# Kernel tuning notes

Hardware: AMD Instinct MI355X
Metric: run time of the kernel (lower is better)

The kernel has to match this reference:

```python
import jax, jax.numpy as jnp
import numpy as np

NUM_ITERS = 2  # quasi-DEER fixed-point iterations (module default num_iters=2)


def _affine_scan(A, b):
    """Parallel first-order linear recurrence h_t = A_t*h_{t-1} + b_t along axis=1.
    A, b: (B, T, H). Equivalent to torch accelerated-scan after removing pow-2 padding."""
    def comb(l, r):
        A1, b1 = l
        A2, b2 = r
        return A2 * A1, A2 * b1 + b2
    return jax.lax.associative_scan(comb, (A, b), axis=1)[1]


def _run_direction(x, W_in, b_in, W_rec, U_z, b_u, num_iters):
    """quasi-DEER evaluation of a MinRNN layer.
    x: (B, T, d_in). Returns states (B, T, H). Initial state h0 = 0 (hx=None)."""
    B, T, _ = x.shape
    H = b_in.shape[0]
    dtype = x.dtype
    h0 = jnp.zeros((B, H), dtype)
    diag_rec = jnp.diagonal(W_rec)  # (H,)
    # z depends only on the input, not on the state -> precompute once.
    z = jnp.tanh(jnp.einsum('bti,hi->bth', x, W_in) + b_in)  # (B, T, H)
    z0, z_rest = z[:, 0], z[:, 1:]
    states = jnp.zeros((B, T, H), dtype)
    for _ in range(num_iters):
        h_prev = states[:, :-1]  # (B, T-1, H), paired with inputs[:,1:]
        u = jax.nn.sigmoid(jnp.einsum('bth,gh->btg', h_prev, W_rec)
                           + jnp.einsum('bth,gh->btg', z_rest, U_z) + b_u)
        fs = u * h_prev + (1.0 - u) * z_rest                      # cell output f
        As = u + (h_prev - z_rest) * u * (1.0 - u) * diag_rec     # diagonal Jacobian
        bs = fs - As * h_prev
        u0 = jax.nn.sigmoid(h0 @ W_rec.T + z0 @ U_z.T + b_u)
        b0 = u0 * h0 + (1.0 - u0) * z0                            # f(x_0, h0)
        A = jnp.concatenate([jnp.zeros_like(b0)[:, None], As], axis=1)  # A0 = 0
        b = jnp.concatenate([b0[:, None], bs], axis=1)
        states = _affine_scan(A, b)
    return states


def _prnn_forward(input, Wf_in, bf_in, Wf_rec, Uf_z, bf_u,
                  Wb_in, bb_in, Wb_rec, Ub_z, bb_u):
    fwd = _run_direction(input, Wf_in, bf_in, Wf_rec, Uf_z, bf_u, NUM_ITERS)
    bwd = _run_direction(input[:, ::-1], Wb_in, bb_in, Wb_rec, Ub_z, bb_u, NUM_ITERS)[:, ::-1]
    output = jnp.concatenate([fwd, bwd], axis=2)      # (B, T, 2H)
    h_n = jnp.stack([fwd[:, -1], bwd[:, 0]])          # (2, B, H)
    return output, h_n


def setup_inputs() -> dict:
    key = jax.random.key(0)
    ks = jax.random.split(key, 12)
    B, T, D_IN, H = 8, 8192, 256, 256
    def minrnn_params(k0, k1, k2, d_in, h):
        kw, kr, ku = k0, k1, k2
        return dict(
            W_in=jax.random.normal(kw, (h, d_in), jnp.float32) / d_in ** 0.5,
            b_in=jnp.zeros((h,), jnp.float32),
            W_rec=jax.random.normal(kr, (h, h), jnp.float32) / h ** 0.5,
            U_z=jax.random.normal(ku, (h, h), jnp.float32) / h ** 0.5,
            b_u=jnp.zeros((h,), jnp.float32),
        )
    pf = minrnn_params(ks[0], ks[1], ks[2], D_IN, H)
    pb = minrnn_params(ks[3], ks[4], ks[5], D_IN, H)
    return {
        'input': jax.random.normal(ks[6], (B, T, D_IN), jnp.float32),
        'Wf_in': pf['W_in'], 'bf_in': pf['b_in'], 'Wf_rec': pf['W_rec'],
        'Uf_z': pf['U_z'], 'bf_u': pf['b_u'],
        'Wb_in': pb['W_in'], 'bb_in': pb['b_in'], 'Wb_rec': pb['W_rec'],
        'Ub_z': pb['U_z'], 'bb_u': pb['b_u'],
    }


def reference(input, Wf_in, bf_in, Wf_rec, Uf_z, bf_u,
              Wb_in, bb_in, Wb_rec, Ub_z, bb_u):
    return _prnn_forward(input, Wf_in, bf_in, Wf_rec, Uf_z, bf_u,
                         Wb_in, bb_in, Wb_rec, Ub_z, bb_u)
```

## Files before the change

### kernel.cpp

```cpp
#include <hip/hip_runtime.h>
#include <stdint.h>

typedef unsigned short u16;
typedef __attribute__((ext_vector_type(8))) short short8v;
typedef __attribute__((ext_vector_type(4))) short short4v;
typedef __attribute__((ext_vector_type(4))) float f32x4;

#define B_ 8
#define T_ 8192
#define H_ 256
#define M_ 65536
#define MH 16777216
#define NCH 256
#define CHL 32
#define NCHAN 4096

__device__ __forceinline__ u16 f2bf(float f) {
  union { float f; uint32_t u; } v; v.f = f;
  return (u16)((v.u + 0x7FFFu + ((v.u >> 16) & 1u)) >> 16);
}
__device__ __forceinline__ float bf2f(u16 s) {
  union { uint32_t u; float f; } v; v.u = ((uint32_t)s) << 16;
  return v.f;
}
__device__ __forceinline__ float sigm(float x) {
  return __fdividef(1.0f, 1.0f + __expf(-x));
}
__device__ __forceinline__ float tanhfast(float x) {
  return 1.0f - __fdividef(2.0f, __expf(2.0f * x) + 1.0f);
}

__device__ __forceinline__ void compute_Ab(float zf, float ag, float hp, float dr,
                                           float& Aa, float& bb) {
  const float u = sigm(ag);
  const float g = u * (1.f - u) * dr;
  Aa = u + (hp - zf) * g;
  bb = u * hp + (1.f - u) * zf - Aa * hp;
}

__global__ __launch_bounds__(256) void prep_kernel(
    const float* __restrict__ x, u16* __restrict__ xf,
    const float* __restrict__ w0, const float* __restrict__ w1, const float* __restrict__ w2,
    const float* __restrict__ w3, const float* __restrict__ w4, const float* __restrict__ w5,
    u16* __restrict__ wbf) {
  const int bx = blockIdx.x;
  const float* src;
  u16* dst;
  size_t i;
  if (bx < 8192) {
    i = ((size_t)bx * 256 + threadIdx.x) * 8;
    src = x; dst = xf;
  } else {
    const int r = bx - 8192;
    const int wsel = r >> 5, blk = r & 31;
    src = (wsel == 0) ? w0 : (wsel == 1) ? w1 : (wsel == 2) ? w2
        : (wsel == 3) ? w3 : (wsel == 4) ? w4 : w5;
    dst = wbf + (size_t)wsel * 65536;
    i = ((size_t)blk * 256 + threadIdx.x) * 8;
  }
  const float4* s4 = (const float4*)(src + i);
  float4 a = s4[0], b = s4[1];
  short8v o;
  o[0] = (short)f2bf(a.x); o[1] = (short)f2bf(a.y);
  o[2] = (short)f2bf(a.z); o[3] = (short)f2bf(a.w);
  o[4] = (short)f2bf(b.x); o[5] = (short)f2bf(b.y);
  o[6] = (short)f2bf(b.z); o[7] = (short)f2bf(b.w);
  *(short8v*)(dst + i) = o;
}

__device__ __forceinline__ void g2l16(const void* g, void* l) {
  __builtin_amdgcn_global_load_lds((const __attribute__((address_space(1))) void*)g,
                                   (__attribute__((address_space(3))) void*)l, 16, 0, 0);
}
__device__ __forceinline__ int ltswz(int row, int col16) {
  return row * 128 + (col16 ^ ((row & 7) << 4));
}

template <int EPI, int REVZ, int FUSE>
__global__ __launch_bounds__(256) void gemm_k(const u16* __restrict__ A, size_t strideA,
                                              const u16* __restrict__ Bw,
                                              const float* __restrict__ bias0,
                                              const float* __restrict__ bias1,
                                              const u16* addm, u16* C,
                                              const u16* zp_g,
                                              const float* __restrict__ Wf_rec,
                                              const float* __restrict__ Wb_rec,
                                              float* __restrict__ Pout,
                                              float* __restrict__ qout) {
  __shared__ __align__(16) char lds[32768];
  char* ldsA = lds;
  char* ldsB = lds + 16384;
  const int bz = blockIdx.z;
  A += (size_t)bz * strideA;
  Bw += (size_t)bz * 196608;
  C += (size_t)bz * (size_t)MH;
  if (EPI == 3) addm += (size_t)bz * (size_t)MH;
  if (FUSE == 2) zp_g += (size_t)bz * (size_t)MH;
  const float* bias = bz ? bias1 : bias0;

  const int tid = threadIdx.x;
  const int l = tid & 63, w = tid >> 6;
  const int tm = blockIdx.x, tn = blockIdx.y;
  const int m0 = (w >> 1) * 64, n0 = (w & 1) * 64;
  const int wbase = w * 1024;
  const bool rev = REVZ && (bz == 1);

  f32x4 vzero = {0.f, 0.f, 0.f, 0.f};
  f32x4 acc[4][4];
#pragma unroll
  for (int i = 0; i < 4; ++i)
#pragma unroll
    for (int j = 0; j < 4; ++j) acc[i][j] = vzero;

#pragma unroll
  for (int k0 = 0; k0 < 256; k0 += 64) {
#pragma unroll
    for (int is = 0; is < 4; ++is) {
      const int o = is * 4096 + tid * 16;
      const int row = o >> 7;
      const int cb = (o & 127) ^ ((row & 7) << 4);
      int rA = tm * 128 + row;
      if (rev) { int bb = rA >> 13; int t = rA & 8191; rA = (bb << 13) + (8191 - t); }
      const char* gA = (const char*)A + (size_t)rA * 512 + k0 * 2 + cb;
      g2l16(gA, ldsA + is * 4096 + wbase);
      const int rB = tn * 128 + row;
      const char* gB = (const char*)Bw + (size_t)rB * 512 + k0 * 2 + cb;
      g2l16(gB, ldsB + is * 4096 + wbase);
    }
    __syncthreads();
#pragma unroll
    for (int ks = 0; ks < 2; ++ks) {
      const int colb = (ks * 64 + (l >> 4) * 16) ^ ((l & 7) << 4);
      short8v av[4], bv[4];
#pragma unroll
      for (int i = 0; i < 4; ++i) {
        av[i] = *(const short8v*)(ldsA + (m0 + i * 16 + (l & 15)) * 128 + colb);
        bv[i] = *(const short8v*)(ldsB + (n0 + i * 16 + (l & 15)) * 128 + colb);
      }
#pragma unroll
      for (int i = 0; i < 4; ++i)
#pragma unroll
        for (int j = 0; j < 4; ++j)
          acc[i][j] = __builtin_amdgcn_mfma_f32_16x16x32_bf16(av[i], bv[j], acc[i][j], 0, 0, 0);
    }
    __syncthreads();
  }

  u16* lt = (u16*)lds;
  const int colL = n0 + (l & 15);
  const int rowL0 = m0 + ((l >> 4) << 2);
#pragma unroll
  for (int j = 0; j < 4; ++j) {
    const int cl = colL + j * 16;
    const int cg = tn * 128 + cl;
    const float bv = (EPI == 3) ? 0.f : bias[cg];
#pragma unroll
    for (int i = 0; i < 4; ++i)
#pragma unroll
      for (int r = 0; r < 4; ++r) {
        const int rl = rowL0 + i * 16 + r;
        float xv = acc[i][j][r] + bv;
        if (EPI == 3) xv += bf2f(addm[(size_t)(tm * 128 + rl) * 256 + cg]);
        if (EPI == 0) xv = tanhfast(xv);
        lt[ltswz(rl, cl)] = f2bf(xv);
      }
  }
  __syncthreads();
#pragma unroll
  for (int itr = 0; itr < 8; ++itr) {
    const int rl = w * 32 + itr * 4 + (l >> 4);
    const int c16 = ((l & 15) * 8) ^ ((rl & 7) << 4);
    short8v v = *(const short8v*)(lt + rl * 128 + c16);
    *(short8v*)((char*)C + (size_t)(tm * 128 + rl) * 512 + tn * 256 + (l & 15) * 16) = v;
  }

  if (FUSE) {
    const int cl = tid & 127;
    const int hg = tn * 128 + cl;
    const float dr = (bz ? Wb_rec : Wf_rec)[hg * 257];
    const int bb = (tm * 128) >> 13;
    const int c0 = ((tm * 128) & 8191) >> 5;
    const int ch = (bz * 8 + bb) * 256 + hg;
#pragma unroll
    for (int cc = 0; cc < 2; ++cc) {
      const int clc = (tid >> 7) * 2 + cc;
      float Pv = 1.f, qv = 0.f;
      const size_t gbase = (size_t)(tm * 128 + clc * CHL) * 256 + hg;
#pragma unroll 4
      for (int it = 0; it < CHL; ++it) {
        const float ag = bf2f(lt[ltswz(clc * CHL + it, cl)]);
        float zf, hp;
        if (FUSE == 1) { zf = bf2f(A[gbase + (size_t)it * 256]); hp = 0.f; }
        else { zf = bf2f(zp_g[gbase + (size_t)it * 256]); hp = bf2f(A[gbase + (size_t)it * 256]); }
        float Aa, bbv;
        compute_Ab(zf, ag, hp, dr, Aa, bbv);
        qv = Aa * qv + bbv;
        Pv *= Aa;
      }
      Pout[(size_t)(c0 + clc) * NCHAN + ch] = Pv;
      qout[(size_t)(c0 + clc) * NCHAN + ch] = qv;
    }
  }
}

__global__ __launch_bounds__(256) void scan_p2_kernel(const float* __restrict__ P,
                                                      const float* __restrict__ q,
                                                      float* __restrict__ hstart) {
  const int ch = blockIdx.x * 256 + threadIdx.x;
  float hs = 0.f;
#pragma unroll 8
  for (int c = 0; c < NCH; ++c) {
    hstart[c * NCHAN + ch] = hs;
    hs = P[c * NCHAN + ch] * hs + q[c * NCHAN + ch];
  }
}

template <int ITER>
__global__ __launch_bounds__(256) void scan_p3_kernel(
    const u16* __restrict__ zb, const u16* __restrict__ zub,
    const u16* __restrict__ s1b,
    const float* __restrict__ Wf_rec, const float* __restrict__ Wb_rec,
    const float* __restrict__ hstart,
    u16* __restrict__ s1out, float* __restrict__ out, float* __restrict__ hn) {
  const int wid = blockIdx.x * 4 + (threadIdx.x >> 6);
  const int lane = threadIdx.x & 63;
  const int c = wid & (NCH - 1);
  const int tmp = wid >> 8;
  const int b = tmp & 7;
  const int d = tmp >> 3;
  const int h0 = lane * 4;
  const float* Wr = d ? Wb_rec : Wf_rec;
  float dr[4];
#pragma unroll
  for (int j = 0; j < 4; ++j) dr[j] = Wr[(h0 + j) * 257];
  const size_t off = (size_t)d * MH + ((size_t)b * T_ + (size_t)c * CHL) * H_ + h0;
  const u16* zp = zb + off;
  const u16* zup = zub + off;
  const u16* s1p = s1b + off;
  const int ch0 = (d * 8 + b) * 256 + h0;
  f32x4 h4 = *(const f32x4*)(hstart + (size_t)c * NCHAN + ch0);
  float hc[4] = {h4[0], h4[1], h4[2], h4[3]};
  if (ITER == 1 && c == 0) {
    *(short4v*)(s1out + off) = (short4v){0, 0, 0, 0};
  }
#pragma unroll 4
  for (int it = 0; it < CHL; ++it) {
    const size_t ix = (size_t)it * H_;
    short4v z4 = *(const short4v*)(zp + ix);
    short4v a4 = *(const short4v*)(zup + ix);
    short4v s4 = {0, 0, 0, 0};
    if (ITER == 2) s4 = *(const short4v*)(s1p + ix);
#pragma unroll
    for (int j = 0; j < 4; ++j) {
      const float zf = bf2f((u16)z4[j]);
      const float ag = bf2f((u16)a4[j]);
      const float hp = (ITER == 2) ? bf2f((u16)s4[j]) : 0.f;
      float Aa, bb;
      compute_Ab(zf, ag, hp, dr[j], Aa, bb);
      hc[j] = Aa * hc[j] + bb;
    }
    const int t = c * CHL + it;
    if (ITER == 1) {
      if (t < T_ - 1) {
        short4v o = {(short)f2bf(hc[0]), (short)f2bf(hc[1]),
                     (short)f2bf(hc[2]), (short)f2bf(hc[3])};
        *(short4v*)(s1out + off + ix + H_) = o;
      }
    } else {
      const size_t to = (d == 0) ? ((size_t)b * T_ + t) * 512 + h0
                                 : ((size_t)b * T_ + (T_ - 1 - t)) * 512 + 256 + h0;
      *(f32x4*)(out + to) = (f32x4){hc[0], hc[1], hc[2], hc[3]};
      if (t == T_ - 1)
        *(f32x4*)(hn + (size_t)(d * 8 + b) * 256 + h0) = (f32x4){hc[0], hc[1], hc[2], hc[3]};
    }
  }
}

extern "C" void kernel_launch(void* const* d_in, const int* in_sizes, int n_in,
                              void* d_out, int out_size, void* d_ws, size_t ws_size,
                              hipStream_t stream) {
  const float* x      = (const float*)d_in[0];
  const float* Wf_in  = (const float*)d_in[1];
  const float* bf_in  = (const float*)d_in[2];
  const float* Wf_rec = (const float*)d_in[3];
  const float* Uf_z   = (const float*)d_in[4];
  const float* bf_u   = (const float*)d_in[5];
  const float* Wb_in  = (const float*)d_in[6];
  const float* bb_in  = (const float*)d_in[7];
  const float* Wb_rec = (const float*)d_in[8];
  const float* Ub_z   = (const float*)d_in[9];
  const float* bb_u   = (const float*)d_in[10];

  char* ws = (char*)d_ws;
  const size_t BF = 33554432;
  u16* xf  = (u16*)(ws + 0 * BF);
  u16* z0  = (u16*)(ws + 1 * BF);
  u16* zu0 = (u16*)(ws + 3 * BF);
  u16* s10 = (u16*)(ws + 5 * BF);
  u16* wbf = (u16*)(ws + 7 * BF);
  char* pb = ws + 7 * BF + 1048576;
  float* Pbuf = (float*)(pb);
  float* qbuf = (float*)(pb + 4194304);
  float* hst  = (float*)(pb + 8388608);
  (void)ws_size; (void)in_sizes; (void)n_in; (void)out_size;

  float* outp = (float*)d_out;
  float* hnp  = outp + (size_t)33554432;

  dim3 gg(512, 2, 2);

  prep_kernel<<<8384, 256, 0, stream>>>(x, xf, Wf_in, Uf_z, Wf_rec, Wb_in, Ub_z, Wb_rec, wbf);

  gemm_k<0, 1, 0><<<gg, 256, 0, stream>>>(xf, 0, wbf + 0 * 65536, bf_in, bb_in,
                                          nullptr, z0, nullptr, nullptr, nullptr,
                                          nullptr, nullptr);
  gemm_k<1, 0, 1><<<gg, 256, 0, stream>>>(z0, MH, wbf + 1 * 65536, bf_u, bb_u,
                                          nullptr, zu0, nullptr, Wf_rec, Wb_rec,
                                          Pbuf, qbuf);

  scan_p2_kernel<<<16, 256, 0, stream>>>(Pbuf, qbuf, hst);
  scan_p3_kernel<1><<<1024, 256, 0, stream>>>(z0, zu0, s10, Wf_rec, Wb_rec, hst,
                                              s10, nullptr, nullptr);

  gemm_k<3, 0, 2><<<gg, 256, 0, stream>>>(s10, MH, wbf + 2 * 65536, nullptr, nullptr,
                                          zu0, zu0, z0, Wf_rec, Wb_rec,
                                          Pbuf, qbuf);

  scan_p2_kernel<<<16, 256, 0, stream>>>(Pbuf, qbuf, hst);
  scan_p3_kernel<2><<<1024, 256, 0, stream>>>(z0, zu0, s10, Wf_rec, Wb_rec, hst,
                                              nullptr, outp, hnp);
}
```

Measured before the change: 334.8 us.

## Double-buffer GEMM LDS tiles and remap blocks across XCDs

The GEMM K-loop now uses two LDS buffers (64KB total), prefetching the next K slice with global_load_lds while MFMAs consume the current one, synchronised by explicit vmcnt waits and raw barriers. The grid is flattened to 1024 blocks, with the block index decoded so that consecutive blocks spread M tiles across the 8 XCDs and the two N tiles of one M tile share an XCD for L2 reuse. The aim is to hide global load latency and improve cache locality. The larger LDS footprint lowers occupancy per CU.

```diff
diff --git a/kernel.cpp b/kernel.cpp
--- a/kernel.cpp
+++ b/kernel.cpp
@@ -87,9 +87,7 @@
                                               const float* __restrict__ Wb_rec,
                                               float* __restrict__ Pout,
                                               float* __restrict__ qout) {
-  __shared__ __align__(16) char lds[32768];
-  char* ldsA = lds;
-  char* ldsB = lds + 16384;
+  __shared__ __align__(16) char lds[65536];
   const int bz = blockIdx.z;
   A += (size_t)bz * strideA;
   Bw += (size_t)bz * 196608;
@@ -100,20 +98,16 @@
 
   const int tid = threadIdx.x;
   const int l = tid & 63, w = tid >> 6;
-  const int tm = blockIdx.x, tn = blockIdx.y;
+  const int dd = blockIdx.x;
+  const int xcd = dd & 7;
+  const int rem = dd >> 3;
+  const int tn = rem & 1;
+  const int tm = (rem >> 1) * 8 + xcd;
   const int m0 = (w >> 1) * 64, n0 = (w & 1) * 64;
   const int wbase = w * 1024;
   const bool rev = REVZ && (bz == 1);
 
-  f32x4 vzero = {0.f, 0.f, 0.f, 0.f};
-  f32x4 acc[4][4];
-#pragma unroll
-  for (int i = 0; i < 4; ++i)
-#pragma unroll
-    for (int j = 0; j < 4; ++j) acc[i][j] = vzero;
-
-#pragma unroll
-  for (int k0 = 0; k0 < 256; k0 += 64) {
+  auto stage = [&](int p, int k0) {
 #pragma unroll
     for (int is = 0; is < 4; ++is) {
       const int o = is * 4096 + tid * 16;
@@ -122,20 +116,39 @@
       int rA = tm * 128 + row;
       if (rev) { int bb = rA >> 13; int t = rA & 8191; rA = (bb << 13) + (8191 - t); }
       const char* gA = (const char*)A + (size_t)rA * 512 + k0 * 2 + cb;
-      g2l16(gA, ldsA + is * 4096 + wbase);
+      g2l16(gA, lds + p * 32768 + is * 4096 + wbase);
       const int rB = tn * 128 + row;
       const char* gB = (const char*)Bw + (size_t)rB * 512 + k0 * 2 + cb;
-      g2l16(gB, ldsB + is * 4096 + wbase);
-    }
-    __syncthreads();
+      g2l16(gB, lds + p * 32768 + 16384 + is * 4096 + wbase);
+    }
+  };
+
+  f32x4 vzero = {0.f, 0.f, 0.f, 0.f};
+  f32x4 acc[4][4];
+#pragma unroll
+  for (int i = 0; i < 4; ++i)
+#pragma unroll
+    for (int j = 0; j < 4; ++j) acc[i][j] = vzero;
+
+  stage(0, 0);
+#pragma unroll
+  for (int k = 0; k < 4; ++k) {
+    const int p = k & 1;
+    if (k < 3) {
+      stage(p ^ 1, (k + 1) * 64);
+      asm volatile("s_waitcnt vmcnt(8)" ::: "memory");
+    } else {
+      asm volatile("s_waitcnt vmcnt(0)" ::: "memory");
+    }
+    __builtin_amdgcn_s_barrier();
 #pragma unroll
     for (int ks = 0; ks < 2; ++ks) {
       const int colb = (ks * 64 + (l >> 4) * 16) ^ ((l & 7) << 4);
       short8v av[4], bv[4];
 #pragma unroll
       for (int i = 0; i < 4; ++i) {
-        av[i] = *(const short8v*)(ldsA + (m0 + i * 16 + (l & 15)) * 128 + colb);
-        bv[i] = *(const short8v*)(ldsB + (n0 + i * 16 + (l & 15)) * 128 + colb);
+        av[i] = *(const short8v*)(lds + p * 32768 + (m0 + i * 16 + (l & 15)) * 128 + colb);
+        bv[i] = *(const short8v*)(lds + p * 32768 + 16384 + (n0 + i * 16 + (l & 15)) * 128 + colb);
       }
 #pragma unroll
       for (int i = 0; i < 4; ++i)
@@ -143,7 +156,7 @@
         for (int j = 0; j < 4; ++j)
           acc[i][j] = __builtin_amdgcn_mfma_f32_16x16x32_bf16(av[i], bv[j], acc[i][j], 0, 0, 0);
     }
-    __syncthreads();
+    __builtin_amdgcn_s_barrier();
   }
 
   u16* lt = (u16*)lds;
@@ -307,7 +320,7 @@
   float* outp = (float*)d_out;
   float* hnp  = outp + (size_t)33554432;
 
-  dim3 gg(512, 2, 2);
+  dim3 gg(1024, 1, 2);
 
   prep_kernel<<<8384, 256, 0, stream>>>(x, xf, Wf_in, Uf_z, Wf_rec, Wb_in, Ub_z, Wb_rec, wbf);
 
```

Measured after the change: 334.2 us. About the same (-0.2%).

## Fuse z/zu GEMMs and iteration-1 scan fixup into GEMM kernels

Applied to the files above, without the earlier changes.

Replaces the two separate z and zu GEMMs with one kernel. Each block computes a 64-row tile of z across all 256 columns, keeps it in LDS, and immediately multiplies it by U_z, then computes the chunk prefix products from LDS. The first-iteration scan fixup (scan_p3<1>) is merged into the W_rec GEMM kernel, which rebuilds s1 in LDS and feeds it straight into the MFMA. This removes several full-size bf16 round trips through global memory and two launches. In exchange the serial per-chunk recurrence now runs inside a GEMM block, and the larger LDS footprint may lower occupancy.

```diff
diff --git a/kernel.cpp b/kernel.cpp
--- a/kernel.cpp
+++ b/kernel.cpp
@@ -36,6 +36,14 @@
   const float g = u * (1.f - u) * dr;
   Aa = u + (hp - zf) * g;
   bb = u * hp + (1.f - u) * zf - Aa * hp;
+}
+
+__device__ __forceinline__ void g2l16(const void* g, void* l) {
+  __builtin_amdgcn_global_load_lds((const __attribute__((address_space(1))) void*)g,
+                                   (__attribute__((address_space(3))) void*)l, 16, 0, 0);
+}
+__device__ __forceinline__ int zts(int row, int col) {
+  return row * 256 + ((((col >> 3) ^ (row & 7)) << 3) | (col & 7));
 }
 
 __global__ __launch_bounds__(256) void prep_kernel(
@@ -68,42 +76,25 @@
   *(short8v*)(dst + i) = o;
 }
 
-__device__ __forceinline__ void g2l16(const void* g, void* l) {
-  __builtin_amdgcn_global_load_lds((const __attribute__((address_space(1))) void*)g,
-                                   (__attribute__((address_space(3))) void*)l, 16, 0, 0);
-}
-__device__ __forceinline__ int ltswz(int row, int col16) {
-  return row * 128 + (col16 ^ ((row & 7) << 4));
-}
-
-template <int EPI, int REVZ, int FUSE>
-__global__ __launch_bounds__(256) void gemm_k(const u16* __restrict__ A, size_t strideA,
-                                              const u16* __restrict__ Bw,
-                                              const float* __restrict__ bias0,
-                                              const float* __restrict__ bias1,
-                                              const u16* addm, u16* C,
-                                              const u16* zp_g,
-                                              const float* __restrict__ Wf_rec,
-                                              const float* __restrict__ Wb_rec,
-                                              float* __restrict__ Pout,
-                                              float* __restrict__ qout) {
-  __shared__ __align__(16) char lds[32768];
-  char* ldsA = lds;
-  char* ldsB = lds + 16384;
-  const int bz = blockIdx.z;
-  A += (size_t)bz * strideA;
-  Bw += (size_t)bz * 196608;
-  C += (size_t)bz * (size_t)MH;
-  if (EPI == 3) addm += (size_t)bz * (size_t)MH;
-  if (FUSE == 2) zp_g += (size_t)bz * (size_t)MH;
-  const float* bias = bz ? bias1 : bias0;
-
-  const int tid = threadIdx.x;
-  const int l = tid & 63, w = tid >> 6;
-  const int tm = blockIdx.x, tn = blockIdx.y;
-  const int m0 = (w >> 1) * 64, n0 = (w & 1) * 64;
-  const int wbase = w * 1024;
-  const bool rev = REVZ && (bz == 1);
+__global__ __launch_bounds__(256) void zzu_k(
+    const u16* __restrict__ xf, const u16* __restrict__ wbf,
+    const float* __restrict__ bin0, const float* __restrict__ bin1,
+    const float* __restrict__ bu0, const float* __restrict__ bu1,
+    const float* __restrict__ Wf_rec, const float* __restrict__ Wb_rec,
+    u16* __restrict__ zout, u16* __restrict__ zuout,
+    float* __restrict__ Pout, float* __restrict__ qout) {
+  __shared__ __align__(16) char lds[65536];
+  const int dir = blockIdx.z;
+  const int tm = blockIdx.x;
+  const char* Win = (const char*)(wbf + (size_t)dir * 196608);
+  const char* Uz  = (const char*)(wbf + (size_t)dir * 196608 + 65536);
+  const float* bin = dir ? bin1 : bin0;
+  const float* bu  = dir ? bu1 : bu0;
+  const int tid = threadIdx.x, l = tid & 63, w = tid >> 6;
+  const int n0 = w * 64;
+  const size_t zoff = (size_t)dir * MH;
+  u16* zt  = (u16*)(lds + 32768);
+  u16* zut = (u16*)lds;
 
   f32x4 vzero = {0.f, 0.f, 0.f, 0.f};
   f32x4 acc[4][4];
@@ -115,27 +106,31 @@
 #pragma unroll
   for (int k0 = 0; k0 < 256; k0 += 64) {
 #pragma unroll
-    for (int is = 0; is < 4; ++is) {
+    for (int is = 0; is < 2; ++is) {
       const int o = is * 4096 + tid * 16;
       const int row = o >> 7;
       const int cb = (o & 127) ^ ((row & 7) << 4);
-      int rA = tm * 128 + row;
-      if (rev) { int bb = rA >> 13; int t = rA & 8191; rA = (bb << 13) + (8191 - t); }
-      const char* gA = (const char*)A + (size_t)rA * 512 + k0 * 2 + cb;
-      g2l16(gA, ldsA + is * 4096 + wbase);
-      const int rB = tn * 128 + row;
-      const char* gB = (const char*)Bw + (size_t)rB * 512 + k0 * 2 + cb;
-      g2l16(gB, ldsB + is * 4096 + wbase);
-    }
-    __syncthreads();
-#pragma unroll
-    for (int ks = 0; ks < 2; ++ks) {
-      const int colb = (ks * 64 + (l >> 4) * 16) ^ ((l & 7) << 4);
+      int rA = tm * 64 + row;
+      if (dir) { int bb = rA >> 13; int t = rA & 8191; rA = (bb << 13) + (8191 - t); }
+      g2l16((const char*)xf + (size_t)rA * 512 + k0 * 2 + cb,
+            lds + 32768 + is * 4096 + w * 1024);
+    }
+#pragma unroll
+    for (int is = 0; is < 8; ++is) {
+      const int o = is * 4096 + tid * 16;
+      const int row = o >> 7;
+      const int cb = (o & 127) ^ ((row & 7) << 4);
+      g2l16(Win + (size_t)row * 512 + k0 * 2 + cb, lds + is * 4096 + w * 1024);
+    }
+    __syncthreads();
+#pragma unroll
+    for (int kk = 0; kk < 2; ++kk) {
+      const int colb = (kk * 64 + (l >> 4) * 16) ^ ((l & 7) << 4);
       short8v av[4], bv[4];
 #pragma unroll
       for (int i = 0; i < 4; ++i) {
-        av[i] = *(const short8v*)(ldsA + (m0 + i * 16 + (l & 15)) * 128 + colb);
-        bv[i] = *(const short8v*)(ldsB + (n0 + i * 16 + (l & 15)) * 128 + colb);
+        av[i] = *(const short8v*)(lds + 32768 + (i * 16 + (l & 15)) * 128 + colb);
+        bv[i] = *(const short8v*)(lds + (n0 + i * 16 + (l & 15)) * 128 + colb);
       }
 #pragma unroll
       for (int i = 0; i < 4; ++i)
@@ -146,60 +141,247 @@
     __syncthreads();
   }
 
-  u16* lt = (u16*)lds;
-  const int colL = n0 + (l & 15);
-  const int rowL0 = m0 + ((l >> 4) << 2);
 #pragma unroll
   for (int j = 0; j < 4; ++j) {
-    const int cl = colL + j * 16;
-    const int cg = tn * 128 + cl;
-    const float bv = (EPI == 3) ? 0.f : bias[cg];
+    const int col = n0 + j * 16 + (l & 15);
+    const float bv = bin[col];
 #pragma unroll
     for (int i = 0; i < 4; ++i)
 #pragma unroll
       for (int r = 0; r < 4; ++r) {
-        const int rl = rowL0 + i * 16 + r;
-        float xv = acc[i][j][r] + bv;
-        if (EPI == 3) xv += bf2f(addm[(size_t)(tm * 128 + rl) * 256 + cg]);
-        if (EPI == 0) xv = tanhfast(xv);
-        lt[ltswz(rl, cl)] = f2bf(xv);
+        const int row = (l >> 4) * 4 + i * 16 + r;
+        zt[zts(row, col)] = f2bf(tanhfast(acc[i][j][r] + bv));
       }
   }
   __syncthreads();
-#pragma unroll
-  for (int itr = 0; itr < 8; ++itr) {
-    const int rl = w * 32 + itr * 4 + (l >> 4);
-    const int c16 = ((l & 15) * 8) ^ ((rl & 7) << 4);
-    short8v v = *(const short8v*)(lt + rl * 128 + c16);
-    *(short8v*)((char*)C + (size_t)(tm * 128 + rl) * 512 + tn * 256 + (l & 15) * 16) = v;
-  }
-
-  if (FUSE) {
-    const int cl = tid & 127;
-    const int hg = tn * 128 + cl;
-    const float dr = (bz ? Wb_rec : Wf_rec)[hg * 257];
-    const int bb = (tm * 128) >> 13;
-    const int c0 = ((tm * 128) & 8191) >> 5;
-    const int ch = (bz * 8 + bb) * 256 + hg;
+
+  {
+    const int row = tid >> 2;
+    const int ub = (tid & 3) * 8;
+    char* g = (char*)(zout + zoff) + (size_t)(tm * 64 + row) * 512;
+#pragma unroll
+    for (int q = 0; q < 8; ++q) {
+      const int u = ub + q;
+      short8v v = *(const short8v*)((const char*)zt + row * 512 + ((u ^ (row & 7)) << 4));
+      *(short8v*)(g + u * 16) = v;
+    }
+  }
+
+#pragma unroll
+  for (int i = 0; i < 4; ++i)
+#pragma unroll
+    for (int j = 0; j < 4; ++j) acc[i][j] = vzero;
+#pragma unroll
+  for (int k0 = 0; k0 < 256; k0 += 64) {
+#pragma unroll
+    for (int is = 0; is < 8; ++is) {
+      const int o = is * 4096 + tid * 16;
+      const int row = o >> 7;
+      const int cb = (o & 127) ^ ((row & 7) << 4);
+      g2l16(Uz + (size_t)row * 512 + k0 * 2 + cb, lds + is * 4096 + w * 1024);
+    }
+    __syncthreads();
+#pragma unroll
+    for (int kk = 0; kk < 2; ++kk) {
+      short8v av[4], bv[4];
+#pragma unroll
+      for (int i = 0; i < 4; ++i) {
+        const int row = i * 16 + (l & 15);
+        const int u = (k0 >> 3) + kk * 4 + (l >> 4);
+        av[i] = *(const short8v*)((const char*)zt + row * 512 + ((u ^ (row & 7)) << 4));
+        const int colb = (kk * 64 + (l >> 4) * 16) ^ ((l & 7) << 4);
+        bv[i] = *(const short8v*)(lds + (n0 + i * 16 + (l & 15)) * 128 + colb);
+      }
+#pragma unroll
+      for (int i = 0; i < 4; ++i)
+#pragma unroll
+        for (int j = 0; j < 4; ++j)
+          acc[i][j] = __builtin_amdgcn_mfma_f32_16x16x32_bf16(av[i], bv[j], acc[i][j], 0, 0, 0);
+    }
+    __syncthreads();
+  }
+
+#pragma unroll
+  for (int j = 0; j < 4; ++j) {
+    const int col = n0 + j * 16 + (l & 15);
+    const float bv = bu[col];
+#pragma unroll
+    for (int i = 0; i < 4; ++i)
+#pragma unroll
+      for (int r = 0; r < 4; ++r) {
+        const int row = (l >> 4) * 4 + i * 16 + r;
+        zut[zts(row, col)] = f2bf(acc[i][j][r] + bv);
+      }
+  }
+  __syncthreads();
+
+  {
+    const int row = tid >> 2;
+    const int ub = (tid & 3) * 8;
+    char* g = (char*)(zuout + zoff) + (size_t)(tm * 64 + row) * 512;
+#pragma unroll
+    for (int q = 0; q < 8; ++q) {
+      const int u = ub + q;
+      short8v v = *(const short8v*)((const char*)zut + row * 512 + ((u ^ (row & 7)) << 4));
+      *(short8v*)(g + u * 16) = v;
+    }
+  }
+
+  {
+    const int h = tid;
+    const float dr = (dir ? Wb_rec : Wf_rec)[h * 257];
+    const int b = tm >> 7;
+    const int c0 = (tm & 127) * 2;
+    const int ch = (dir * 8 + b) * 256 + h;
 #pragma unroll
     for (int cc = 0; cc < 2; ++cc) {
-      const int clc = (tid >> 7) * 2 + cc;
       float Pv = 1.f, qv = 0.f;
-      const size_t gbase = (size_t)(tm * 128 + clc * CHL) * 256 + hg;
 #pragma unroll 4
       for (int it = 0; it < CHL; ++it) {
-        const float ag = bf2f(lt[ltswz(clc * CHL + it, cl)]);
-        float zf, hp;
-        if (FUSE == 1) { zf = bf2f(A[gbase + (size_t)it * 256]); hp = 0.f; }
-        else { zf = bf2f(zp_g[gbase + (size_t)it * 256]); hp = bf2f(A[gbase + (size_t)it * 256]); }
+        const int row = cc * 32 + it;
+        const float zf = bf2f(zt[zts(row, h)]);
+        const float ag = bf2f(zut[zts(row, h)]);
         float Aa, bbv;
-        compute_Ab(zf, ag, hp, dr, Aa, bbv);
+        compute_Ab(zf, ag, 0.f, dr, Aa, bbv);
         qv = Aa * qv + bbv;
         Pv *= Aa;
       }
-      Pout[(size_t)(c0 + clc) * NCHAN + ch] = Pv;
-      qout[(size_t)(c0 + clc) * NCHAN + ch] = qv;
-    }
+      Pout[(size_t)(c0 + cc) * NCHAN + ch] = Pv;
+      qout[(size_t)(c0 + cc) * NCHAN + ch] = qv;
+    }
+  }
+}
+
+__global__ __launch_bounds__(256) void s1zuh_k(
+    const u16* __restrict__ zb, u16* __restrict__ zub,
+    const u16* __restrict__ wbf,
+    const float* __restrict__ Wf_rec, const float* __restrict__ Wb_rec,
+    const float* __restrict__ hst,
+    u16* __restrict__ s1out, float* __restrict__ Pout, float* __restrict__ qout) {
+  __shared__ __align__(16) char lds[65536];
+  const int dir = blockIdx.z;
+  const int tm = blockIdx.x;
+  const char* Wr = (const char*)(wbf + (size_t)dir * 196608 + 131072);
+  const int tid = threadIdx.x, l = tid & 63, w = tid >> 6;
+  const int n0 = w * 64;
+  const size_t zoff = (size_t)dir * MH;
+  u16* s1t = (u16*)(lds + 32768);
+  u16* zht = (u16*)lds;
+
+  const int h = tid;
+  const float dr = (dir ? Wb_rec : Wf_rec)[h * 257];
+  const int b = tm >> 7;
+  const int c0 = (tm & 127) * 2;
+  const int ch = (dir * 8 + b) * 256 + h;
+
+  s1t[zts(0, h)] = f2bf(hst[(size_t)c0 * NCHAN + ch]);
+#pragma unroll
+  for (int cc = 0; cc < 2; ++cc) {
+    float hcur = hst[(size_t)(c0 + cc) * NCHAN + ch];
+#pragma unroll 4
+    for (int it = 0; it < CHL; ++it) {
+      const size_t g = (size_t)(tm * 64 + cc * 32 + it) * 256 + h;
+      const float zf = bf2f(zb[zoff + g]);
+      const float ag = bf2f(zub[zoff + g]);
+      float Aa, bbv;
+      compute_Ab(zf, ag, 0.f, dr, Aa, bbv);
+      hcur = Aa * hcur + bbv;
+      const int rr = cc * 32 + it + 1;
+      if (rr < 64) s1t[zts(rr, h)] = f2bf(hcur);
+    }
+  }
+  __syncthreads();
+
+  {
+    const int row = tid >> 2;
+    const int ub = (tid & 3) * 8;
+    char* g = (char*)(s1out + zoff) + (size_t)(tm * 64 + row) * 512;
+#pragma unroll
+    for (int q = 0; q < 8; ++q) {
+      const int u = ub + q;
+      short8v v = *(const short8v*)((const char*)s1t + row * 512 + ((u ^ (row & 7)) << 4));
+      *(short8v*)(g + u * 16) = v;
+    }
+  }
+
+  f32x4 vzero = {0.f, 0.f, 0.f, 0.f};
+  f32x4 acc[4][4];
+#pragma unroll
+  for (int i = 0; i < 4; ++i)
+#pragma unroll
+    for (int j = 0; j < 4; ++j) acc[i][j] = vzero;
+#pragma unroll
+  for (int k0 = 0; k0 < 256; k0 += 64) {
+#pragma unroll
+    for (int is = 0; is < 8; ++is) {
+      const int o = is * 4096 + tid * 16;
+      const int row = o >> 7;
+      const int cb = (o & 127) ^ ((row & 7) << 4);
+      g2l16(Wr + (size_t)row * 512 + k0 * 2 + cb, lds + is * 4096 + w * 1024);
+    }
+    __syncthreads();
+#pragma unroll
+    for (int kk = 0; kk < 2; ++kk) {
+      short8v av[4], bv[4];
+#pragma unroll
+      for (int i = 0; i < 4; ++i) {
+        const int row = i * 16 + (l & 15);
+        const int u = (k0 >> 3) + kk * 4 + (l >> 4);
+        av[i] = *(const short8v*)((const char*)s1t + row * 512 + ((u ^ (row & 7)) << 4));
+        const int colb = (kk * 64 + (l >> 4) * 16) ^ ((l & 7) << 4);
+        bv[i] = *(const short8v*)(lds + (n0 + i * 16 + (l & 15)) * 128 + colb);
+      }
+#pragma unroll
+      for (int i = 0; i < 4; ++i)
+#pragma unroll
+        for (int j = 0; j < 4; ++j)
+          acc[i][j] = __builtin_amdgcn_mfma_f32_16x16x32_bf16(av[i], bv[j], acc[i][j], 0, 0, 0);
+    }
+    __syncthreads();
+  }
+
+#pragma unroll
+  for (int j = 0; j < 4; ++j) {
+    const int col = n0 + j * 16 + (l & 15);
+#pragma unroll
+    for (int i = 0; i < 4; ++i)
+#pragma unroll
+      for (int r = 0; r < 4; ++r) {
+        const int row = (l >> 4) * 4 + i * 16 + r;
+        const float xv = acc[i][j][r] + bf2f(zub[zoff + (size_t)(tm * 64 + row) * 256 + col]);
+        zht[zts(row, col)] = f2bf(xv);
+      }
+  }
+  __syncthreads();
+
+  {
+    const int row = tid >> 2;
+    const int ub = (tid & 3) * 8;
+    char* g = (char*)(zub + zoff) + (size_t)(tm * 64 + row) * 512;
+#pragma unroll
+    for (int q = 0; q < 8; ++q) {
+      const int u = ub + q;
+      short8v v = *(const short8v*)((const char*)zht + row * 512 + ((u ^ (row & 7)) << 4));
+      *(short8v*)(g + u * 16) = v;
+    }
+  }
+
+#pragma unroll
+  for (int cc = 0; cc < 2; ++cc) {
+    float Pv = 1.f, qv = 0.f;
+#pragma unroll 4
+    for (int it = 0; it < CHL; ++it) {
+      const int row = cc * 32 + it;
+      const float zf = bf2f(zb[zoff + (size_t)(tm * 64 + row) * 256 + h]);
+      const float hp = bf2f(s1t[zts(row, h)]);
+      const float ag = bf2f(zht[zts(row, h)]);
+      float Aa, bbv;
+      compute_Ab(zf, ag, hp, dr, Aa, bbv);
+      qv = Aa * qv + bbv;
+      Pv *= Aa;
+    }
+    Pout[(size_t)(c0 + cc) * NCHAN + ch] = Pv;
+    qout[(size_t)(c0 + cc) * NCHAN + ch] = qv;
   }
 }
 
@@ -215,13 +397,12 @@
   }
 }
 
-template <int ITER>
 __global__ __launch_bounds__(256) void scan_p3_kernel(
     const u16* __restrict__ zb, const u16* __restrict__ zub,
     const u16* __restrict__ s1b,
     const float* __restrict__ Wf_rec, const float* __restrict__ Wb_rec,
     const float* __restrict__ hstart,
-    u16* __restrict__ s1out, float* __restrict__ out, float* __restrict__ hn) {
+    float* __restrict__ out, float* __restrict__ hn) {
   const int wid = blockIdx.x * 4 + (threadIdx.x >> 6);
   const int lane = threadIdx.x & 63;
   const int c = wid & (NCH - 1);
@@ -240,39 +421,27 @@
   const int ch0 = (d * 8 + b) * 256 + h0;
   f32x4 h4 = *(const f32x4*)(hstart + (size_t)c * NCHAN + ch0);
   float hc[4] = {h4[0], h4[1], h4[2], h4[3]};
-  if (ITER == 1 && c == 0) {
-    *(short4v*)(s1out + off) = (short4v){0, 0, 0, 0};
-  }
 #pragma unroll 4
   for (int it = 0; it < CHL; ++it) {
     const size_t ix = (size_t)it * H_;
     short4v z4 = *(const short4v*)(zp + ix);
     short4v a4 = *(const short4v*)(zup + ix);
-    short4v s4 = {0, 0, 0, 0};
-    if (ITER == 2) s4 = *(const short4v*)(s1p + ix);
+    short4v s4 = *(const short4v*)(s1p + ix);
 #pragma unroll
     for (int j = 0; j < 4; ++j) {
       const float zf = bf2f((u16)z4[j]);
       const float ag = bf2f((u16)a4[j]);
-      const float hp = (ITER == 2) ? bf2f((u16)s4[j]) : 0.f;
+      const float hp = bf2f((u16)s4[j]);
       float Aa, bb;
       compute_Ab(zf, ag, hp, dr[j], Aa, bb);
       hc[j] = Aa * hc[j] + bb;
     }
     const int t = c * CHL + it;
-    if (ITER == 1) {
-      if (t < T_ - 1) {
-        short4v o = {(short)f2bf(hc[0]), (short)f2bf(hc[1]),
-                     (short)f2bf(hc[2]), (short)f2bf(hc[3])};
-        *(short4v*)(s1out + off + ix + H_) = o;
-      }
-    } else {
-      const size_t to = (d == 0) ? ((size_t)b * T_ + t) * 512 + h0
-                                 : ((size_t)b * T_ + (T_ - 1 - t)) * 512 + 256 + h0;
-      *(f32x4*)(out + to) = (f32x4){hc[0], hc[1], hc[2], hc[3]};
-      if (t == T_ - 1)
-        *(f32x4*)(hn + (size_t)(d * 8 + b) * 256 + h0) = (f32x4){hc[0], hc[1], hc[2], hc[3]};
-    }
+    const size_t to = (d == 0) ? ((size_t)b * T_ + t) * 512 + h0
+                               : ((size_t)b * T_ + (T_ - 1 - t)) * 512 + 256 + h0;
+    *(f32x4*)(out + to) = (f32x4){hc[0], hc[1], hc[2], hc[3]};
+    if (t == T_ - 1)
+      *(f32x4*)(hn + (size_t)(d * 8 + b) * 256 + h0) = (f32x4){hc[0], hc[1], hc[2], hc[3]};
   }
 }
 
@@ -307,26 +476,16 @@
   float* outp = (float*)d_out;
   float* hnp  = outp + (size_t)33554432;
 
-  dim3 gg(512, 2, 2);
+  dim3 gt(1024, 1, 2);
 
   prep_kernel<<<8384, 256, 0, stream>>>(x, xf, Wf_in, Uf_z, Wf_rec, Wb_in, Ub_z, Wb_rec, wbf);
 
-  gemm_k<0, 1, 0><<<gg, 256, 0, stream>>>(xf, 0, wbf + 0 * 65536, bf_in, bb_in,
-                                          nullptr, z0, nullptr, nullptr, nullptr,
-                                          nullptr, nullptr);
-  gemm_k<1, 0, 1><<<gg, 256, 0, stream>>>(z0, MH, wbf + 1 * 65536, bf_u, bb_u,
-                                          nullptr, zu0, nullptr, Wf_rec, Wb_rec,
-                                          Pbuf, qbuf);
-
+  zzu_k<<<gt, 256, 0, stream>>>(xf, wbf, bf_in, bb_in, bf_u, bb_u, Wf_rec, Wb_rec,
+                                z0, zu0, Pbuf, qbuf);
   scan_p2_kernel<<<16, 256, 0, stream>>>(Pbuf, qbuf, hst);
-  scan_p3_kernel<1><<<1024, 256, 0, stream>>>(z0, zu0, s10, Wf_rec, Wb_rec, hst,
-                                              s10, nullptr, nullptr);
-
-  gemm_k<3, 0, 2><<<gg, 256, 0, stream>>>(s10, MH, wbf + 2 * 65536, nullptr, nullptr,
-                                          zu0, zu0, z0, Wf_rec, Wb_rec,
-                                          Pbuf, qbuf);
-
+
+  s1zuh_k<<<gt, 256, 0, stream>>>(z0, zu0, wbf, Wf_rec, Wb_rec, hst, s10, Pbuf, qbuf);
   scan_p2_kernel<<<16, 256, 0, stream>>>(Pbuf, qbuf, hst);
-  scan_p3_kernel<2><<<1024, 256, 0, stream>>>(z0, zu0, s10, Wf_rec, Wb_rec, hst,
-                                              nullptr, outp, hnp);
-}
+
+  scan_p3_kernel<<<1024, 256, 0, stream>>>(z0, zu0, s10, Wf_rec, Wb_rec, hst, outp, hnp);
+}
```

After: 356.3 us. 1.06x slower.
